# Performance work log

Hardware: AMD Instinct MI355X
Metric: run time of the kernel (lower is better)

Reference implementation:

```python
import jax, jax.numpy as jnp
import numpy as np

N_HEAD = 16
D_MODEL = 1024
MAX_LEN = 1024  # must equal D_MODEL for the original module's final conv to typecheck
B = 8
L = 1024


def _conv1x1(x, W, b):
    # Conv1d kernel_size=1: [B, C_in, L] -> [B, C_out, L]
    return jnp.einsum('oc,bcl->bol', W, x) + b[None, :, None]


def setup_inputs() -> dict:
    key = jax.random.key(0)
    ks = jax.random.split(key, 11)
    s = 0.02
    return {
        'q': jax.random.normal(ks[0], (B, D_MODEL, L), jnp.float32),
        'k': jax.random.normal(ks[1], (B, D_MODEL, L), jnp.float32),
        'v': jax.random.normal(ks[2], (B, D_MODEL, L), jnp.float32),
        'Wq': jax.random.normal(ks[3], (MAX_LEN, D_MODEL), jnp.float32) * s,
        'bq': jnp.zeros((MAX_LEN,), jnp.float32),
        'Wk': jax.random.normal(ks[4], (MAX_LEN, D_MODEL), jnp.float32) * s,
        'bk': jnp.zeros((MAX_LEN,), jnp.float32),
        'Wv': jax.random.normal(ks[5], (MAX_LEN, D_MODEL), jnp.float32) * s,
        'bv': jnp.zeros((MAX_LEN,), jnp.float32),
        'Wo': jax.random.normal(ks[6], (D_MODEL, D_MODEL), jnp.float32) * s,
        'bo': jnp.zeros((D_MODEL,), jnp.float32),
    }


def reference(q, k, v, Wq, bq, Wk, bk, Wv, bv, Wo, bo):
    # 1x1-conv projections: [B, d_model, L] -> [B, max_len, L]
    qp = _conv1x1(q, Wq, bq)
    kp = _conv1x1(k, Wk, bk)
    vp = _conv1x1(v, Wv, bv)

    b_, ml, l = qp.shape
    dt = l // N_HEAD  # d_tensor
    # project(): raw view splitting the LAST axis blockwise (no transpose!)
    qh = qp.reshape(b_, N_HEAD, ml, dt)
    kh = kp.reshape(b_, N_HEAD, ml, dt)
    vh = vp.reshape(b_, N_HEAD, ml, dt)

    # ScaleDotProductAttention: k_t is a raw VIEW to [b, h, dt, ml], not a transpose
    k_t = kh.reshape(b_, N_HEAD, dt, ml)
    score = jnp.matmul(qh, k_t) / jnp.sqrt(jnp.float32(dt))  # [b, h, ml, ml]
    # nn.Softmax() with dim=None on a 4D tensor -> softmax over dim=1 (legacy torch)
    score = jax.nn.softmax(score, axis=1)
    out = jnp.matmul(score, vh)  # [b, h, ml, dt]

    # concat(): raw view back to [b, ml, l]
    out = out.reshape(b_, ml, l)
    # final 1x1 conv (requires ml == d_model)
    return _conv1x1(out, Wo, bo)
```

## Files before the change

### kernel.cpp

```cpp
#include <hip/hip_runtime.h>
#include <hip/hip_bf16.h>
#include <cstdint>

using bf16 = __hip_bfloat16;
typedef __bf16 bf16x8 __attribute__((ext_vector_type(8)));
typedef float f32x4 __attribute__((ext_vector_type(4)));

#define DEV static __device__ __forceinline__

DEV float toF(float x) { return x; }
DEV float toF(bf16 x) { return __bfloat162float(x); }

DEV float lo2f(unsigned int u) { return __builtin_bit_cast(float, u << 16); }
DEV float hi2f(unsigned int u) { return __builtin_bit_cast(float, u & 0xffff0000u); }
DEV unsigned int pkr(float lo, float hi) {
  return ((__builtin_bit_cast(unsigned int, lo) + 0x8000u) >> 16) |
         ((__builtin_bit_cast(unsigned int, hi) + 0x8000u) & 0xffff0000u);
}
DEV float fexp2(float x) {
  float r;
  asm("v_exp_f32 %0, %1" : "=v"(r) : "v"(x));
  return r;
}
DEV float frcp(float x) {
  float r;
  asm("v_rcp_f32 %0, %1" : "=v"(r) : "v"(x));
  return r;
}

DEV void gload_lds16(const void* g, void* l) {
  __builtin_amdgcn_global_load_lds(
      (const __attribute__((address_space(1))) unsigned int*)g,
      (__attribute__((address_space(3))) unsigned int*)l, 16, 0, 0);
}

template <int BM, int BN, int MODE, bool BIAS_COL>
__launch_bounds__(256, 2)
__global__ void gemm_bt(const bf16* __restrict__ A, long long sA,
                        const bf16* __restrict__ B, long long sB,
                        void* __restrict__ Cv, long long sC,
                        const float* __restrict__ bias,
                        int K, int lda, int ldb, int ldc, float alpha) {
  constexpr int BK = 32;
  constexpr int TX = 1024 / BN;
  __shared__ bf16 ldsA[BM * BK];
  __shared__ bf16 ldsB[BN * BK];
  const int tid = threadIdx.x;
  const int wave = tid >> 6, lane = tid & 63;
  const int bid = blockIdx.x;
  const long long z = bid & 7;
  const int t = bid >> 3;
  A += z * sA;
  B += z * sB;
  const int m0 = (t / TX) * BM, n0 = (t % TX) * BN;

  constexpr int WM = BM / 2, WN = BN / 2;
  constexpr int MR = WM / 16, NR = WN / 16;
  const int wm = (wave >> 1) * WM, wn = (wave & 1) * WN;
  const int lrow = lane & 15;
  const int kb = (lane >> 4) * 8;

  f32x4 acc[MR][NR] = {};

  for (int k0 = 0; k0 < K; k0 += BK) {
#pragma unroll
    for (int r = 0; r < BM / 64; ++r) {
      int c = r * 256 + tid;
      int row = c >> 2, sub = c & 3;
      gload_lds16(A + (long long)(m0 + row) * lda + k0 + sub * 8,
                  (void*)(ldsA + (r * 256 + wave * 64) * 8));
    }
#pragma unroll
    for (int r = 0; r < BN / 64; ++r) {
      int c = r * 256 + tid;
      int row = c >> 2, sub = c & 3;
      gload_lds16(B + (long long)(n0 + row) * ldb + k0 + sub * 8,
                  (void*)(ldsB + (r * 256 + wave * 64) * 8));
    }
    __syncthreads();

    bf16x8 af[MR], bfr[NR];
#pragma unroll
    for (int i = 0; i < MR; ++i)
      af[i] = *(const bf16x8*)&ldsA[(wm + i * 16 + lrow) * BK + kb];
#pragma unroll
    for (int j = 0; j < NR; ++j)
      bfr[j] = *(const bf16x8*)&ldsB[(wn + j * 16 + lrow) * BK + kb];
#pragma unroll
    for (int i = 0; i < MR; ++i)
#pragma unroll
      for (int j = 0; j < NR; ++j)
        acc[i][j] =
            __builtin_amdgcn_mfma_f32_16x16x32_bf16(af[i], bfr[j], acc[i][j], 0, 0, 0);
    __syncthreads();
  }

  const int r4 = (lane >> 4) * 4;
#pragma unroll
  for (int i = 0; i < MR; ++i) {
#pragma unroll
    for (int j = 0; j < NR; ++j) {
#pragma unroll
      for (int r = 0; r < 4; ++r) {
        int grow = m0 + wm + i * 16 + r4 + r;
        int gcol = n0 + wn + j * 16 + lrow;
        float vv = acc[i][j][r];
        if (bias) vv += BIAS_COL ? bias[gcol] : bias[grow];
        vv *= alpha;
        if constexpr (MODE == 0) {
          ((float*)Cv)[z * sC + (long long)grow * ldc + gcol] = vv;
        } else if constexpr (MODE == 1) {
          ((bf16*)Cv)[z * sC + (long long)grow * ldc + gcol] = __float2bfloat16(vv);
        } else if constexpr (MODE == 2) {
          long long idx = ((long long)(gcol >> 6) << 16) + grow * 64 + (gcol & 63);
          ((bf16*)Cv)[z * sC + idx] = __float2bfloat16(vv);
        } else {
          int mm = ((grow & 63) << 4) | (gcol >> 6);
          long long idx = ((long long)(grow >> 6) << 16) + ((mm >> 5) << 11) +
                          ((gcol & 63) << 5) + (mm & 31);
          ((bf16*)Cv)[z * sC + idx] = __float2bfloat16(vv);
        }
      }
    }
  }
}

__launch_bounds__(1024, 4)
__global__ void fused_attn(const bf16* __restrict__ qp,
                           const bf16* __restrict__ kph,
                           const bf16* __restrict__ vptc,
                           bf16* __restrict__ aout) {
  __shared__ unsigned int SP[16 * 32 * 68];
  const int bid = blockIdx.x;
  const int bb = bid & 7, mt = bid >> 3;
  const int tid = threadIdx.x;
  const int w = tid >> 6, lane = tid & 63;
  const int l15 = lane & 15, g = lane >> 4;

  const bf16* Qb = qp + ((size_t)bb << 20);
  const bf16* Kb = kph + ((size_t)bb << 20) + ((size_t)w << 16);
  const bf16* Vb = vptc + ((size_t)bb << 20) + ((size_t)w << 16);
  bf16* Ob = aout + ((size_t)bb << 20);

  bf16x8 qf[2][2];
#pragma unroll
  for (int mf = 0; mf < 2; ++mf)
#pragma unroll
    for (int kc = 0; kc < 2; ++kc)
      qf[mf][kc] = *(const bf16x8*)(Qb + ((size_t)w << 16) +
                                    (mt * 32 + mf * 16 + l15) * 64 + kc * 32 + g * 8);

  f32x4 oacc[2][4] = {};
  const unsigned int hrow = w * 2176;

  for (int it = 0; it < 8; ++it) {
    const int n0 = it * 128;
#pragma unroll
    for (int mmf = 0; mmf < 8; ++mmf) {
      const bf16* kr = Kb + (size_t)(n0 + mmf * 16 + l15) * 64 + g * 8;
      bf16x8 k0 = *(const bf16x8*)kr;
      bf16x8 k1 = *(const bf16x8*)(kr + 32);
      f32x4 sa = {}, sb = {};
      __builtin_amdgcn_s_setprio(1);
      sa = __builtin_amdgcn_mfma_f32_16x16x32_bf16(k0, qf[0][0], sa, 0, 0, 0);
      sa = __builtin_amdgcn_mfma_f32_16x16x32_bf16(k1, qf[0][1], sa, 0, 0, 0);
      sb = __builtin_amdgcn_mfma_f32_16x16x32_bf16(k0, qf[1][0], sb, 0, 0, 0);
      sb = __builtin_amdgcn_mfma_f32_16x16x32_bf16(k1, qf[1][1], sb, 0, 0, 0);
      __builtin_amdgcn_s_setprio(0);
      uint2 ua, ub;
      ua.x = pkr(sa[0], sa[1]);
      ua.y = pkr(sa[2], sa[3]);
      ub.x = pkr(sb[0], sb[1]);
      ub.y = pkr(sb[2], sb[3]);
      *(uint2*)&SP[hrow + l15 * 68 + mmf * 8 + g * 2] = ua;
      *(uint2*)&SP[hrow + (16 + l15) * 68 + mmf * 8 + g * 2] = ub;
    }
    __syncthreads();
#pragma unroll
    for (int pi = 0; pi < 2; ++pi) {
      const int p = tid + pi * 1024;
      const int base = (p >> 6) * 68 + (p & 63);
      float el[16], eh[16];
#pragma unroll
      for (int h = 0; h < 16; ++h) {
        unsigned int u = SP[h * 2176 + base];
        el[h] = fexp2(lo2f(u));
        eh[h] = fexp2(hi2f(u));
      }
      float sl = (((el[0] + el[1]) + (el[2] + el[3])) + ((el[4] + el[5]) + (el[6] + el[7]))) +
                 (((el[8] + el[9]) + (el[10] + el[11])) + ((el[12] + el[13]) + (el[14] + el[15])));
      float sh = (((eh[0] + eh[1]) + (eh[2] + eh[3])) + ((eh[4] + eh[5]) + (eh[6] + eh[7]))) +
                 (((eh[8] + eh[9]) + (eh[10] + eh[11])) + ((eh[12] + eh[13]) + (eh[14] + eh[15])));
      float il = frcp(sl), ih = frcp(sh);
#pragma unroll
      for (int h = 0; h < 16; ++h)
        SP[h * 2176 + base] = pkr(el[h] * il, eh[h] * ih);
    }
    __syncthreads();
#pragma unroll
    for (int c = 0; c < 4; ++c) {
      uint4 pa0 = *(const uint4*)&SP[hrow + l15 * 68 + c * 16 + g * 4];
      uint4 pa1 = *(const uint4*)&SP[hrow + (16 + l15) * 68 + c * 16 + g * 4];
      bf16x8 p0 = __builtin_bit_cast(bf16x8, pa0);
      bf16x8 p1 = __builtin_bit_cast(bf16x8, pa1);
      const bf16* vb = Vb + ((it * 4 + c) << 11) + g * 8;
      __builtin_amdgcn_s_setprio(1);
#pragma unroll
      for (int dj = 0; dj < 4; ++dj) {
        bf16x8 vf = *(const bf16x8*)(vb + (dj * 16 + l15) * 32);
        oacc[0][dj] = __builtin_amdgcn_mfma_f32_16x16x32_bf16(p0, vf, oacc[0][dj], 0, 0, 0);
        oacc[1][dj] = __builtin_amdgcn_mfma_f32_16x16x32_bf16(p1, vf, oacc[1][dj], 0, 0, 0);
      }
      __builtin_amdgcn_s_setprio(0);
    }
  }
#pragma unroll
  for (int mf = 0; mf < 2; ++mf)
#pragma unroll
    for (int dj = 0; dj < 4; ++dj)
#pragma unroll
      for (int r = 0; r < 4; ++r)
        Ob[((size_t)w << 16) + (size_t)(mt * 32 + mf * 16 + g * 4 + r) * 64 +
           dj * 16 + l15] = __float2bfloat16(oacc[mf][dj][r]);
}

template <typename TIN>
__global__ void transpose_tile(const TIN* __restrict__ in, bf16* __restrict__ out,
                               int R, int C, long long sIn, long long sOut) {
  __shared__ float t[32][33];
  const long long z = blockIdx.z;
  in += z * sIn;
  out += z * sOut;
  const int r0 = blockIdx.y * 32, c0 = blockIdx.x * 32;
  const int tx = threadIdx.x, ty = threadIdx.y;
#pragma unroll
  for (int i = ty; i < 32; i += 8)
    t[i][tx] = toF(in[(long long)(r0 + i) * C + c0 + tx]);
  __syncthreads();
#pragma unroll
  for (int i = ty; i < 32; i += 8)
    out[(long long)(c0 + i) * R + r0 + tx] = __float2bfloat16(t[tx][i]);
}

__global__ void transpose_in3(const float* __restrict__ q, const float* __restrict__ k,
                              const float* __restrict__ v, bf16* __restrict__ qT,
                              bf16* __restrict__ kT, bf16* __restrict__ vT) {
  __shared__ float t[32][33];
  const int z = blockIdx.z, bz = z & 7, which = z >> 3;
  const float* in = (which == 0 ? q : which == 1 ? k : v) + (size_t)bz * 1048576;
  bf16* out = (which == 0 ? qT : which == 1 ? kT : vT) + (size_t)bz * 1048576;
  const int r0 = blockIdx.y * 32, c0 = blockIdx.x * 32;
  const int tx = threadIdx.x, ty = threadIdx.y;
#pragma unroll
  for (int i = ty; i < 32; i += 8)
    t[i][tx] = in[(size_t)(r0 + i) * 1024 + c0 + tx];
  __syncthreads();
#pragma unroll
  for (int i = ty; i < 32; i += 8)
    out[(size_t)(c0 + i) * 1024 + r0 + tx] = __float2bfloat16(t[tx][i]);
}

__global__ void cast4(const float* __restrict__ w0, const float* __restrict__ w1,
                      const float* __restrict__ w2, const float* __restrict__ w3,
                      bf16* __restrict__ o0, bf16* __restrict__ o1,
                      bf16* __restrict__ o2, bf16* __restrict__ o3) {
  const int y = blockIdx.y;
  const float* in = y == 0 ? w0 : y == 1 ? w1 : y == 2 ? w2 : w3;
  bf16* out = y == 0 ? o0 : y == 1 ? o1 : y == 2 ? o2 : o3;
  int i = (blockIdx.x * 256 + threadIdx.x) * 4;
  float4 f = *(const float4*)(in + i);
  out[i + 0] = __float2bfloat16(f.x);
  out[i + 1] = __float2bfloat16(f.y);
  out[i + 2] = __float2bfloat16(f.z);
  out[i + 3] = __float2bfloat16(f.w);
}

extern "C" void kernel_launch(void* const* d_in, const int* in_sizes, int n_in,
                              void* d_out, int out_size, void* d_ws, size_t ws_size,
                              hipStream_t stream) {
  (void)in_sizes; (void)n_in; (void)out_size;
  const float* q  = (const float*)d_in[0];
  const float* k  = (const float*)d_in[1];
  const float* v  = (const float*)d_in[2];
  const float* Wq = (const float*)d_in[3];
  const float* bq = (const float*)d_in[4];
  const float* Wk = (const float*)d_in[5];
  const float* bk = (const float*)d_in[6];
  const float* Wv = (const float*)d_in[7];
  const float* bv = (const float*)d_in[8];
  const float* Wo = (const float*)d_in[9];
  const float* bo = (const float*)d_in[10];
  float* out = (float*)d_out;

  const size_t MB = 1ull << 20;
  if (ws_size < 152 * MB) return;
  char* ws = (char*)d_ws;
  bf16* qp    = (bf16*)(ws + 0 * MB);
  bf16* kph   = (bf16*)(ws + 16 * MB);
  bf16* vptc  = (bf16*)(ws + 32 * MB);
  bf16* aout  = (bf16*)(ws + 48 * MB);
  bf16* aoutT = (bf16*)(ws + 64 * MB);
  bf16* WoB   = (bf16*)(ws + 80 * MB);
  char* scr = ws + 82 * MB;
  bf16* WqB = (bf16*)(scr + 0 * MB);
  bf16* WkB = (bf16*)(scr + 2 * MB);
  bf16* WvB = (bf16*)(scr + 4 * MB);
  bf16* qT  = (bf16*)(scr + 6 * MB);
  bf16* kT  = (bf16*)(scr + 22 * MB);
  bf16* vT  = (bf16*)(scr + 38 * MB);

  const long long M1 = 1048576;
  dim3 tb(32, 8);

  cast4<<<dim3(1024, 4), 256, 0, stream>>>(Wq, Wk, Wv, Wo, WqB, WkB, WvB, WoB);
  transpose_in3<<<dim3(32, 32, 24), tb, 0, stream>>>(q, k, v, qT, kT, vT);
  gemm_bt<128, 128, 1, false><<<512, 256, 0, stream>>>(
      WqB, 0, qT, M1, qp, M1, bq, 1024, 1024, 1024, 1024, 0.18033688f);
  gemm_bt<128, 128, 2, true><<<512, 256, 0, stream>>>(
      kT, M1, WkB, 0, kph, M1, bk, 1024, 1024, 1024, 1024, 1.0f);
  gemm_bt<128, 128, 3, false><<<512, 256, 0, stream>>>(
      WvB, 0, vT, M1, vptc, M1, bv, 1024, 1024, 1024, 1024, 1.0f);

  fused_attn<<<dim3(256), 1024, 0, stream>>>(qp, kph, vptc, aout);

  transpose_tile<bf16><<<dim3(32, 32, 8), tb, 0, stream>>>(aout, aoutT, 1024, 1024, M1, M1);
  gemm_bt<128, 128, 0, false><<<512, 256, 0, stream>>>(
      WoB, 0, aoutT, M1, out, M1, bo, 1024, 1024, 1024, 1024, 1.0f);
}
```

Measured before the change: 339.6 us.

## Merge three projection GEMMs into one launch with smaller tiles; prefetch V fragments

Replaces the three separate projection GEMM launches with one proj3 kernel of 3072 blocks that picks Q/K/V work by block index. Tiles shrink from 128x128 to 128x64 with 4 blocks per CU, so there are more blocks to fill the device, at the cost of less operand reuse per block. The output GEMM uses the same smaller tile. In the attention kernel, the V fragments for the first two chunks are loaded before the softmax barrier to hide global latency, which raises register pressure.

```diff
diff --git a/kernel.cpp b/kernel.cpp
--- a/kernel.cpp
+++ b/kernel.cpp
@@ -34,95 +34,134 @@
       (__attribute__((address_space(3))) unsigned int*)l, 16, 0, 0);
 }
 
-template <int BM, int BN, int MODE, bool BIAS_COL>
-__launch_bounds__(256, 2)
-__global__ void gemm_bt(const bf16* __restrict__ A, long long sA,
-                        const bf16* __restrict__ B, long long sB,
-                        void* __restrict__ Cv, long long sC,
-                        const float* __restrict__ bias,
-                        int K, int lda, int ldb, int ldc, float alpha) {
-  constexpr int BK = 32;
-  constexpr int TX = 1024 / BN;
-  __shared__ bf16 ldsA[BM * BK];
-  __shared__ bf16 ldsB[BN * BK];
+#define GEMM_CORE(A_, lda_, B_, ldb_)                                          \
+  f32x4 acc[4][2] = {};                                                        \
+  {                                                                            \
+    const int wave = tid >> 6, lane = tid & 63;                                \
+    const int wm = (wave >> 1) * 64, wn = (wave & 1) * 32;                     \
+    const int lrow = lane & 15;                                                \
+    const int kb = (lane >> 4) * 8;                                            \
+    for (int k0 = 0; k0 < 1024; k0 += 32) {                                    \
+      _Pragma("unroll") for (int r = 0; r < 2; ++r) {                          \
+        int c = r * 256 + tid;                                                 \
+        int row = c >> 2, sub = c & 3;                                         \
+        gload_lds16(A_ + (long long)(m0 + row) * lda_ + k0 + sub * 8,          \
+                    (void*)(ldsA + (r * 256 + wave * 64) * 8));                \
+      }                                                                        \
+      {                                                                        \
+        int row = tid >> 2, sub = tid & 3;                                     \
+        gload_lds16(B_ + (long long)(n0 + row) * ldb_ + k0 + sub * 8,          \
+                    (void*)(ldsB + (wave * 64) * 8));                          \
+      }                                                                        \
+      __syncthreads();                                                         \
+      bf16x8 af[4], bfr[2];                                                    \
+      _Pragma("unroll") for (int i = 0; i < 4; ++i)                            \
+          af[i] = *(const bf16x8*)&ldsA[(wm + i * 16 + lrow) * 32 + kb];       \
+      _Pragma("unroll") for (int j = 0; j < 2; ++j)                            \
+          bfr[j] = *(const bf16x8*)&ldsB[(wn + j * 16 + lrow) * 32 + kb];      \
+      _Pragma("unroll") for (int i = 0; i < 4; ++i)                            \
+          _Pragma("unroll") for (int j = 0; j < 2; ++j)                        \
+              acc[i][j] = __builtin_amdgcn_mfma_f32_16x16x32_bf16(             \
+                  af[i], bfr[j], acc[i][j], 0, 0, 0);                          \
+      __syncthreads();                                                         \
+    }                                                                          \
+  }
+
+__launch_bounds__(256, 4)
+__global__ void proj3(const bf16* __restrict__ Wq, const bf16* __restrict__ qT,
+                      bf16* __restrict__ qp, const float* __restrict__ bq,
+                      const bf16* __restrict__ kT, const bf16* __restrict__ Wk,
+                      bf16* __restrict__ kph, const float* __restrict__ bk,
+                      const bf16* __restrict__ Wv, const bf16* __restrict__ vT,
+                      bf16* __restrict__ vptc, const float* __restrict__ bv) {
+  __shared__ bf16 ldsA[128 * 32];
+  __shared__ bf16 ldsB[64 * 32];
   const int tid = threadIdx.x;
+  const int bid = blockIdx.x;
+  const int which = bid >> 10, r0b = bid & 1023;
+  const long long z = r0b & 7;
+  const int t = r0b >> 3;
+  const int m0 = (t >> 4) * 128, n0 = (t & 15) * 64;
+  const long long M1 = 1048576;
+
+  const bf16* A;
+  const bf16* B;
+  const float* bias;
+  bf16* C;
+  float alpha;
+  if (which == 0) {
+    A = Wq; B = qT + z * M1; bias = bq; C = qp + z * M1; alpha = 0.18033688f;
+  } else if (which == 1) {
+    A = kT + z * M1; B = Wk; bias = bk; C = kph + z * M1; alpha = 1.0f;
+  } else {
+    A = Wv; B = vT + z * M1; bias = bv; C = vptc + z * M1; alpha = 1.0f;
+  }
+
+  GEMM_CORE(A, 1024, B, 1024)
+
   const int wave = tid >> 6, lane = tid & 63;
-  const int bid = blockIdx.x;
-  const long long z = bid & 7;
-  const int t = bid >> 3;
-  A += z * sA;
-  B += z * sB;
-  const int m0 = (t / TX) * BM, n0 = (t % TX) * BN;
-
-  constexpr int WM = BM / 2, WN = BN / 2;
-  constexpr int MR = WM / 16, NR = WN / 16;
-  const int wm = (wave >> 1) * WM, wn = (wave & 1) * WN;
+  const int wm = (wave >> 1) * 64, wn = (wave & 1) * 32;
   const int lrow = lane & 15;
-  const int kb = (lane >> 4) * 8;
-
-  f32x4 acc[MR][NR] = {};
-
-  for (int k0 = 0; k0 < K; k0 += BK) {
-#pragma unroll
-    for (int r = 0; r < BM / 64; ++r) {
-      int c = r * 256 + tid;
-      int row = c >> 2, sub = c & 3;
-      gload_lds16(A + (long long)(m0 + row) * lda + k0 + sub * 8,
-                  (void*)(ldsA + (r * 256 + wave * 64) * 8));
-    }
-#pragma unroll
-    for (int r = 0; r < BN / 64; ++r) {
-      int c = r * 256 + tid;
-      int row = c >> 2, sub = c & 3;
-      gload_lds16(B + (long long)(n0 + row) * ldb + k0 + sub * 8,
-                  (void*)(ldsB + (r * 256 + wave * 64) * 8));
-    }
-    __syncthreads();
-
-    bf16x8 af[MR], bfr[NR];
-#pragma unroll
-    for (int i = 0; i < MR; ++i)
-      af[i] = *(const bf16x8*)&ldsA[(wm + i * 16 + lrow) * BK + kb];
-#pragma unroll
-    for (int j = 0; j < NR; ++j)
-      bfr[j] = *(const bf16x8*)&ldsB[(wn + j * 16 + lrow) * BK + kb];
-#pragma unroll
-    for (int i = 0; i < MR; ++i)
-#pragma unroll
-      for (int j = 0; j < NR; ++j)
-        acc[i][j] =
-            __builtin_amdgcn_mfma_f32_16x16x32_bf16(af[i], bfr[j], acc[i][j], 0, 0, 0);
-    __syncthreads();
-  }
-
   const int r4 = (lane >> 4) * 4;
 #pragma unroll
-  for (int i = 0; i < MR; ++i) {
-#pragma unroll
-    for (int j = 0; j < NR; ++j) {
+  for (int i = 0; i < 4; ++i) {
+#pragma unroll
+    for (int j = 0; j < 2; ++j) {
 #pragma unroll
       for (int r = 0; r < 4; ++r) {
         int grow = m0 + wm + i * 16 + r4 + r;
         int gcol = n0 + wn + j * 16 + lrow;
         float vv = acc[i][j][r];
-        if (bias) vv += BIAS_COL ? bias[gcol] : bias[grow];
-        vv *= alpha;
-        if constexpr (MODE == 0) {
-          ((float*)Cv)[z * sC + (long long)grow * ldc + gcol] = vv;
-        } else if constexpr (MODE == 1) {
-          ((bf16*)Cv)[z * sC + (long long)grow * ldc + gcol] = __float2bfloat16(vv);
-        } else if constexpr (MODE == 2) {
+        if (which == 0) {
+          vv = (vv + bias[grow]) * alpha;
+          C[(long long)grow * 1024 + gcol] = __float2bfloat16(vv);
+        } else if (which == 1) {
+          vv += bias[gcol];
           long long idx = ((long long)(gcol >> 6) << 16) + grow * 64 + (gcol & 63);
-          ((bf16*)Cv)[z * sC + idx] = __float2bfloat16(vv);
+          C[idx] = __float2bfloat16(vv);
         } else {
+          vv += bias[grow];
           int mm = ((grow & 63) << 4) | (gcol >> 6);
           long long idx = ((long long)(grow >> 6) << 16) + ((mm >> 5) << 11) +
                           ((gcol & 63) << 5) + (mm & 31);
-          ((bf16*)Cv)[z * sC + idx] = __float2bfloat16(vv);
+          C[idx] = __float2bfloat16(vv);
         }
       }
     }
   }
+}
+
+__launch_bounds__(256, 4)
+__global__ void gemm_out(const bf16* __restrict__ Wo, const bf16* __restrict__ aoutT,
+                         float* __restrict__ out, const float* __restrict__ bo) {
+  __shared__ bf16 ldsA[128 * 32];
+  __shared__ bf16 ldsB[64 * 32];
+  const int tid = threadIdx.x;
+  const int bid = blockIdx.x;
+  const long long z = bid & 7;
+  const int t = bid >> 3;
+  const int m0 = (t >> 4) * 128, n0 = (t & 15) * 64;
+  const long long M1 = 1048576;
+  const bf16* A = Wo;
+  const bf16* B = aoutT + z * M1;
+  float* C = out + z * M1;
+
+  GEMM_CORE(A, 1024, B, 1024)
+
+  const int wave = tid >> 6, lane = tid & 63;
+  const int wm = (wave >> 1) * 64, wn = (wave & 1) * 32;
+  const int lrow = lane & 15;
+  const int r4 = (lane >> 4) * 4;
+#pragma unroll
+  for (int i = 0; i < 4; ++i)
+#pragma unroll
+    for (int j = 0; j < 2; ++j)
+#pragma unroll
+      for (int r = 0; r < 4; ++r) {
+        int grow = m0 + wm + i * 16 + r4 + r;
+        int gcol = n0 + wn + j * 16 + lrow;
+        C[(long long)grow * 1024 + gcol] = acc[i][j][r] + bo[grow];
+      }
 }
 
 __launch_bounds__(1024, 4)
@@ -175,6 +214,14 @@
       *(uint2*)&SP[hrow + l15 * 68 + mmf * 8 + g * 2] = ua;
       *(uint2*)&SP[hrow + (16 + l15) * 68 + mmf * 8 + g * 2] = ub;
     }
+    bf16x8 vf01[2][4];
+#pragma unroll
+    for (int c = 0; c < 2; ++c) {
+      const bf16* vb = Vb + ((it * 4 + c) << 11) + g * 8;
+#pragma unroll
+      for (int dj = 0; dj < 4; ++dj)
+        vf01[c][dj] = *(const bf16x8*)(vb + (dj * 16 + l15) * 32);
+    }
     __syncthreads();
 #pragma unroll
     for (int pi = 0; pi < 2; ++pi) {
@@ -207,7 +254,8 @@
       __builtin_amdgcn_s_setprio(1);
 #pragma unroll
       for (int dj = 0; dj < 4; ++dj) {
-        bf16x8 vf = *(const bf16x8*)(vb + (dj * 16 + l15) * 32);
+        bf16x8 vf = (c < 2) ? vf01[c][dj]
+                            : *(const bf16x8*)(vb + (dj * 16 + l15) * 32);
         oacc[0][dj] = __builtin_amdgcn_mfma_f32_16x16x32_bf16(p0, vf, oacc[0][dj], 0, 0, 0);
         oacc[1][dj] = __builtin_amdgcn_mfma_f32_16x16x32_bf16(p1, vf, oacc[1][dj], 0, 0, 0);
       }
@@ -314,16 +362,10 @@
 
   cast4<<<dim3(1024, 4), 256, 0, stream>>>(Wq, Wk, Wv, Wo, WqB, WkB, WvB, WoB);
   transpose_in3<<<dim3(32, 32, 24), tb, 0, stream>>>(q, k, v, qT, kT, vT);
-  gemm_bt<128, 128, 1, false><<<512, 256, 0, stream>>>(
-      WqB, 0, qT, M1, qp, M1, bq, 1024, 1024, 1024, 1024, 0.18033688f);
-  gemm_bt<128, 128, 2, true><<<512, 256, 0, stream>>>(
-      kT, M1, WkB, 0, kph, M1, bk, 1024, 1024, 1024, 1024, 1.0f);
-  gemm_bt<128, 128, 3, false><<<512, 256, 0, stream>>>(
-      WvB, 0, vT, M1, vptc, M1, bv, 1024, 1024, 1024, 1024, 1.0f);
+  proj3<<<3072, 256, 0, stream>>>(WqB, qT, qp, bq, kT, WkB, kph, bk, WvB, vT, vptc, bv);
 
   fused_attn<<<dim3(256), 1024, 0, stream>>>(qp, kph, vptc, aout);
 
   transpose_tile<bf16><<<dim3(32, 32, 8), tb, 0, stream>>>(aout, aoutT, 1024, 1024, M1, M1);
-  gemm_bt<128, 128, 0, false><<<512, 256, 0, stream>>>(
-      WoB, 0, aoutT, M1, out, M1, bo, 1024, 1024, 1024, 1024, 1.0f);
-}
+  gemm_out<<<1024, 256, 0, stream>>>(WoB, aoutT, out, bo);
+}
```

After: 349.6 us. 1.03x slower.

## Split attention reduction dimension across two blocks and sum partials in transpose

Applied to the files above, without the earlier changes.

The fused attention kernel now splits the key/value dimension into two halves handled by separate blocks, doubling the grid to 512 blocks and halving shared memory per block. Each half writes a partial output to its own buffer, and the transpose kernel now adds the two partials before transposing. This targets low occupancy and parallelism with only 256 large blocks, at the cost of an extra output buffer read in the transpose and bf16 rounding of partial sums. This is valid because the softmax is over heads per element, not over the key axis, so the partial sums are exact apart from rounding.

```diff
diff --git a/kernel.cpp b/kernel.cpp
--- a/kernel.cpp
+++ b/kernel.cpp
@@ -125,14 +125,16 @@
   }
 }
 
-__launch_bounds__(1024, 4)
+__launch_bounds__(1024, 8)
 __global__ void fused_attn(const bf16* __restrict__ qp,
                            const bf16* __restrict__ kph,
                            const bf16* __restrict__ vptc,
-                           bf16* __restrict__ aout) {
-  __shared__ unsigned int SP[16 * 32 * 68];
+                           bf16* __restrict__ aoutA,
+                           bf16* __restrict__ aoutB) {
+  __shared__ unsigned int SP[16 * 32 * 34];
   const int bid = blockIdx.x;
-  const int bb = bid & 7, mt = bid >> 3;
+  const int bb = bid & 7;
+  const int mt = (bid >> 3) & 31, half = bid >> 8;
   const int tid = threadIdx.x;
   const int w = tid >> 6, lane = tid & 63;
   const int l15 = lane & 15, g = lane >> 4;
@@ -140,7 +142,7 @@
   const bf16* Qb = qp + ((size_t)bb << 20);
   const bf16* Kb = kph + ((size_t)bb << 20) + ((size_t)w << 16);
   const bf16* Vb = vptc + ((size_t)bb << 20) + ((size_t)w << 16);
-  bf16* Ob = aout + ((size_t)bb << 20);
+  bf16* Ob = (half ? aoutB : aoutA) + ((size_t)bb << 20);
 
   bf16x8 qf[2][2];
 #pragma unroll
@@ -151,13 +153,13 @@
                                     (mt * 32 + mf * 16 + l15) * 64 + kc * 32 + g * 8);
 
   f32x4 oacc[2][4] = {};
-  const unsigned int hrow = w * 2176;
+  const unsigned int hrow = w * 1088;
 
   for (int it = 0; it < 8; ++it) {
-    const int n0 = it * 128;
-#pragma unroll
-    for (int mmf = 0; mmf < 8; ++mmf) {
-      const bf16* kr = Kb + (size_t)(n0 + mmf * 16 + l15) * 64 + g * 8;
+    const int mm0 = half * 512 + it * 64;
+#pragma unroll
+    for (int mmf = 0; mmf < 4; ++mmf) {
+      const bf16* kr = Kb + (size_t)(mm0 + mmf * 16 + l15) * 64 + g * 8;
       bf16x8 k0 = *(const bf16x8*)kr;
       bf16x8 k1 = *(const bf16x8*)(kr + 32);
       f32x4 sa = {}, sb = {};
@@ -172,18 +174,16 @@
       ua.y = pkr(sa[2], sa[3]);
       ub.x = pkr(sb[0], sb[1]);
       ub.y = pkr(sb[2], sb[3]);
-      *(uint2*)&SP[hrow + l15 * 68 + mmf * 8 + g * 2] = ua;
-      *(uint2*)&SP[hrow + (16 + l15) * 68 + mmf * 8 + g * 2] = ub;
+      *(uint2*)&SP[hrow + l15 * 34 + mmf * 8 + g * 2] = ua;
+      *(uint2*)&SP[hrow + (16 + l15) * 34 + mmf * 8 + g * 2] = ub;
     }
     __syncthreads();
-#pragma unroll
-    for (int pi = 0; pi < 2; ++pi) {
-      const int p = tid + pi * 1024;
-      const int base = (p >> 6) * 68 + (p & 63);
+    {
+      const int base = (tid >> 5) * 34 + (tid & 31);
       float el[16], eh[16];
 #pragma unroll
       for (int h = 0; h < 16; ++h) {
-        unsigned int u = SP[h * 2176 + base];
+        unsigned int u = SP[h * 1088 + base];
         el[h] = fexp2(lo2f(u));
         eh[h] = fexp2(hi2f(u));
       }
@@ -194,16 +194,16 @@
       float il = frcp(sl), ih = frcp(sh);
 #pragma unroll
       for (int h = 0; h < 16; ++h)
-        SP[h * 2176 + base] = pkr(el[h] * il, eh[h] * ih);
+        SP[h * 1088 + base] = pkr(el[h] * il, eh[h] * ih);
     }
     __syncthreads();
 #pragma unroll
-    for (int c = 0; c < 4; ++c) {
-      uint4 pa0 = *(const uint4*)&SP[hrow + l15 * 68 + c * 16 + g * 4];
-      uint4 pa1 = *(const uint4*)&SP[hrow + (16 + l15) * 68 + c * 16 + g * 4];
+    for (int c = 0; c < 2; ++c) {
+      uint4 pa0 = *(const uint4*)&SP[hrow + l15 * 34 + c * 16 + g * 4];
+      uint4 pa1 = *(const uint4*)&SP[hrow + (16 + l15) * 34 + c * 16 + g * 4];
       bf16x8 p0 = __builtin_bit_cast(bf16x8, pa0);
       bf16x8 p1 = __builtin_bit_cast(bf16x8, pa1);
-      const bf16* vb = Vb + ((it * 4 + c) << 11) + g * 8;
+      const bf16* vb = Vb + (((mm0 >> 5) + c) << 11) + g * 8;
       __builtin_amdgcn_s_setprio(1);
 #pragma unroll
       for (int dj = 0; dj < 4; ++dj) {
@@ -224,22 +224,24 @@
            dj * 16 + l15] = __float2bfloat16(oacc[mf][dj][r]);
 }
 
-template <typename TIN>
-__global__ void transpose_tile(const TIN* __restrict__ in, bf16* __restrict__ out,
-                               int R, int C, long long sIn, long long sOut) {
+__global__ void transpose_add(const bf16* __restrict__ a, const bf16* __restrict__ b,
+                              bf16* __restrict__ out) {
   __shared__ float t[32][33];
   const long long z = blockIdx.z;
-  in += z * sIn;
-  out += z * sOut;
+  a += z << 20;
+  b += z << 20;
+  out += z << 20;
   const int r0 = blockIdx.y * 32, c0 = blockIdx.x * 32;
   const int tx = threadIdx.x, ty = threadIdx.y;
 #pragma unroll
+  for (int i = ty; i < 32; i += 8) {
+    long long idx = (long long)(r0 + i) * 1024 + c0 + tx;
+    t[i][tx] = toF(a[idx]) + toF(b[idx]);
+  }
+  __syncthreads();
+#pragma unroll
   for (int i = ty; i < 32; i += 8)
-    t[i][tx] = toF(in[(long long)(r0 + i) * C + c0 + tx]);
-  __syncthreads();
-#pragma unroll
-  for (int i = ty; i < 32; i += 8)
-    out[(long long)(c0 + i) * R + r0 + tx] = __float2bfloat16(t[tx][i]);
+    out[(long long)(c0 + i) * 1024 + r0 + tx] = __float2bfloat16(t[tx][i]);
 }
 
 __global__ void transpose_in3(const float* __restrict__ q, const float* __restrict__ k,
@@ -298,8 +300,8 @@
   bf16* qp    = (bf16*)(ws + 0 * MB);
   bf16* kph   = (bf16*)(ws + 16 * MB);
   bf16* vptc  = (bf16*)(ws + 32 * MB);
-  bf16* aout  = (bf16*)(ws + 48 * MB);
-  bf16* aoutT = (bf16*)(ws + 64 * MB);
+  bf16* aoutA = (bf16*)(ws + 48 * MB);
+  bf16* aoutB = (bf16*)(ws + 64 * MB);
   bf16* WoB   = (bf16*)(ws + 80 * MB);
   char* scr = ws + 82 * MB;
   bf16* WqB = (bf16*)(scr + 0 * MB);
@@ -308,6 +310,7 @@
   bf16* qT  = (bf16*)(scr + 6 * MB);
   bf16* kT  = (bf16*)(scr + 22 * MB);
   bf16* vT  = (bf16*)(scr + 38 * MB);
+  bf16* aoutT = (bf16*)(scr + 54 * MB);
 
   const long long M1 = 1048576;
   dim3 tb(32, 8);
@@ -321,9 +324,9 @@
   gemm_bt<128, 128, 3, false><<<512, 256, 0, stream>>>(
       WvB, 0, vT, M1, vptc, M1, bv, 1024, 1024, 1024, 1024, 1.0f);
 
-  fused_attn<<<dim3(256), 1024, 0, stream>>>(qp, kph, vptc, aout);
-
-  transpose_tile<bf16><<<dim3(32, 32, 8), tb, 0, stream>>>(aout, aoutT, 1024, 1024, M1, M1);
+  fused_attn<<<dim3(512), 1024, 0, stream>>>(qp, kph, vptc, aoutA, aoutB);
+
+  transpose_add<<<dim3(32, 32, 8), tb, 0, stream>>>(aoutA, aoutB, aoutT);
   gemm_bt<128, 128, 0, false><<<512, 256, 0, stream>>>(
       WoB, 0, aoutT, M1, out, M1, bo, 1024, 1024, 1024, 1024, 1.0f);
 }
```

After: 409.2 us. 1.21x slower.
